# Performance work log

Measured on AMD Instinct MI355X. Metric: run time of the kernel, lower is better.

## Reference

```python
import jax, jax.numpy as jnp
import numpy as np

CONF_THRES = 0.8
NMS_THRES = 0.4
MAX_DET = 300          # fixed capacity for jit-compatible NMS output
N_BOXES = 262144
N_CLASSES = 80


def xywh2xyxy(x):
    xy, wh = x[..., :2], x[..., 2:4]
    return jnp.concatenate([xy - wh * 0.5, xy + wh * 0.5], axis=-1)


def bbox_iou(box, boxes):
    # one box [4] vs many [N,4]; original uses the +1 pixel-area convention
    x1 = jnp.maximum(box[0], boxes[:, 0])
    y1 = jnp.maximum(box[1], boxes[:, 1])
    x2 = jnp.minimum(box[2], boxes[:, 2])
    y2 = jnp.minimum(box[3], boxes[:, 3])
    inter = jnp.clip(x2 - x1 + 1, 0) * jnp.clip(y2 - y1 + 1, 0)
    a1 = (box[2] - box[0] + 1) * (box[3] - box[1] + 1)
    a2 = (boxes[:, 2] - boxes[:, 0] + 1) * (boxes[:, 3] - boxes[:, 1] + 1)
    return inter / (a1 + a2 - inter + 1e-16)


def nms_single(pred):
    # pred: [N, 85] raw YOLO output for one image
    boxes = xywh2xyxy(pred[:, :4])
    obj = pred[:, 4]
    cls_scores = pred[:, 5:]
    class_conf = cls_scores.max(axis=-1)
    class_pred = jnp.argmax(cls_scores, axis=-1).astype(pred.dtype)
    valid = obj >= CONF_THRES
    score = obj * class_conf
    # sort valid boxes by descending score; invalid pushed to the end
    order = jnp.argsort(jnp.where(valid, -score, jnp.inf))
    det = jnp.concatenate(
        [boxes, obj[:, None], class_conf[:, None], class_pred[:, None]], axis=1
    )[order]  # [N, 7] = x1,y1,x2,y2,obj,class_conf,class_pred
    valid = valid[order]

    def step(valid, _):
        idx = jnp.argmax(valid)            # first still-valid (= highest score)
        any_valid = jnp.any(valid)
        cur = det[idx]
        iou = bbox_iou(cur[:4], det[:, :4])
        invalid = (iou > NMS_THRES) & (det[:, 6] == cur[6]) & valid
        # weighted box merge over the suppressed group (as in original NMS)
        w = jnp.where(invalid, det[:, 4], 0.0)
        merged = (w[:, None] * det[:, :4]).sum(0) / (w.sum() + 1e-16)
        out = jnp.where(any_valid,
                        jnp.concatenate([merged, cur[4:]]),
                        jnp.zeros(7, pred.dtype))
        return valid & ~invalid, (out, any_valid)

    _, (kept, kept_valid) = jax.lax.scan(step, valid, None, length=MAX_DET)
    return kept, kept_valid  # [MAX_DET,7], [MAX_DET]


def setup_inputs() -> dict:
    key = jax.random.key(0)
    detections = jax.random.uniform(key, (1, N_BOXES, 5 + N_CLASSES), dtype=jnp.float32)
    return {"detections": detections}


def reference(detections):
    kept, kv = nms_single(detections[0])
    d = kept[:, 5:]                        # [MAX_DET, 2] = (class_conf, class_pred)
    conf_key = jnp.where(kv, d[:, 0], -jnp.inf)  # padded rows sort to the end
    order = jnp.argsort(conf_key)          # ascending (torch argsort)
    d = d[order][::-1]                     # torch.flip -> descending class_conf
    kv = kv[order][::-1]
    probs = jnp.where(kv, d[:, 0], 0.0)    # self.probs
    ids = d[:, 1][None, :]                 # self.ids, shape [1, MAX_DET]
    return ids, probs
```

## Files before the change

kernel.cpp:

```cpp
#include <hip/hip_runtime.h>

#pragma clang fp contract(off)

#define NBOX 262144
#define NCLS 80
#define ROWS 85
#define CAP 1024
#define NSUB 8
#define SUBCAP 128
#define POOL 8192
#define BPT 4

typedef unsigned long long ull;

__global__ __launch_bounds__(1024) void k_init(int* __restrict__ cnt_pad,
                                               int* __restrict__ pool_count,
                                               int* __restrict__ done_count) {
    const int t = threadIdx.x;
    for (int i = t; i < NCLS * NSUB * 16; i += 1024) cnt_pad[i] = 0;
    if (t == 0) { *pool_count = 0; *done_count = 0; }
}

__global__ __launch_bounds__(256) void k_stage1(const float* __restrict__ det,
                                                int* __restrict__ cnt_pad,
                                                ull* __restrict__ key2,
                                                float* __restrict__ conf2,
                                                float4* __restrict__ box2) {
    __shared__ int s_wl[1024];
    __shared__ float s_obj[1024];
    __shared__ int s_nv;
    const int t = threadIdx.x;
    const int b0 = blockIdx.x * 1024;
    const int sb = blockIdx.x & (NSUB - 1);

    if (t == 0) s_nv = 0;
    __syncthreads();

    float obj[BPT];
    #pragma unroll
    for (int i = 0; i < BPT; i++)
        obj[i] = det[(size_t)(b0 + (i << 8) + t) * ROWS + 4];
    #pragma unroll
    for (int i = 0; i < BPT; i++) {
        if (obj[i] >= 0.8f) {
            int r = atomicAdd(&s_nv, 1);
            s_wl[r] = (i << 8) + t;
            s_obj[r] = obj[i];
        }
    }
    __syncthreads();
    const int nv = s_nv;

    const int grp = t >> 4, c = t & 15;
    const int lane = t & 63;
    #pragma unroll 2
    for (int r0 = 0; r0 < nv; r0 += 16) {
        int widx = r0 + grp;
        if (widx < nv) {
            int b = s_wl[widx];
            const float* p = det + (size_t)(b0 + b) * ROWS;
            float aux = (c < 5) ? p[c] : 0.0f;
            float v0 = p[5 + c];
            float v1 = p[21 + c];
            float v2 = p[37 + c];
            float v3 = p[53 + c];
            float v4 = p[69 + c];
            float mv = v0; int mj = c;
            if (v1 > mv) { mv = v1; mj = 16 + c; }
            if (v2 > mv) { mv = v2; mj = 32 + c; }
            if (v3 > mv) { mv = v3; mj = 48 + c; }
            if (v4 > mv) { mv = v4; mj = 64 + c; }
            #pragma unroll
            for (int off = 8; off; off >>= 1) {
                float ov = __shfl_xor(mv, off);
                int oj = __shfl_xor(mj, off);
                if (ov > mv || (ov == mv && oj < mj)) { mv = ov; mj = oj; }
            }
            int gb = lane & 48;
            float x = __shfl(aux, gb + 0);
            float y = __shfl(aux, gb + 1);
            float w = __shfl(aux, gb + 2);
            float h = __shfl(aux, gb + 3);
            if (c == 0) {
                float ob = s_obj[widx];
                float score = ob * mv;
                float hw = w * 0.5f, hh = h * 0.5f;
                int gi = b0 + b;
                int r = atomicAdd(&cnt_pad[((mj * NSUB + sb) << 4)], 1);
                if (r < SUBCAP) {
                    int pos = (mj << 10) + (sb << 7) + r;
                    key2[pos] = ((ull)(~__float_as_uint(score)) << 32) | (unsigned)gi;
                    conf2[pos] = mv;
                    box2[pos] = make_float4(x - hw, y - hh, x + hw, y + hh);
                }
            }
        }
    }
}

template <int L>
__device__ __forceinline__ int exact_alive(ull (&k)[L]) {
    int a = 0;
    #pragma unroll
    for (int j = 0; j < L; j++) a += (int)__popcll(__ballot(k[j] != ~0ULL));
    return a;
}

template <int L>
__device__ __forceinline__ void pick_loop(ull (&k)[L], float4 (&bx)[L], float (&cf)[L],
                                          float (&ar)[L],
                                          int lane, int& alive, int& np,
                                          ull* pkey, float* pconf, int stopAt) {
    while (alive > stopAt && np < 300) {
        ull lm = k[0]; int lj = 0;
        #pragma unroll
        for (int j = 1; j < L; j++) if (k[j] < lm) { lm = k[j]; lj = j; }
        ull gm = lm;
        #pragma unroll
        for (int off = 32; off; off >>= 1) { ull o = __shfl_xor(gm, off); if (o < gm) gm = o; }
        if (gm == ~0ULL) { alive = 0; break; }
        float4 cb = bx[0]; float cc = cf[0];
        #pragma unroll
        for (int j = 1; j < L; j++) if (j == lj) { cb = bx[j]; cc = cf[j]; }
        ull wb = __ballot(lm == gm);
        int wl2 = (int)__ffsll((long long)wb) - 1;
        cb.x = __shfl(cb.x, wl2); cb.y = __shfl(cb.y, wl2);
        cb.z = __shfl(cb.z, wl2); cb.w = __shfl(cb.w, wl2);
        cc = __shfl(cc, wl2);
        if (lane == 0) { pkey[np] = gm; pconf[np] = cc; }
        np++;
        float a1 = (cb.z - cb.x + 1.0f) * (cb.w - cb.y + 1.0f);
        #pragma unroll
        for (int j = 0; j < L; j++) {
            if (k[j] != ~0ULL) {
                float4 b = bx[j];
                float xx1 = fmaxf(cb.x, b.x), yy1 = fmaxf(cb.y, b.y);
                float xx2 = fminf(cb.z, b.z), yy2 = fminf(cb.w, b.w);
                float iw = xx2 - xx1 + 1.0f, ih = yy2 - yy1 + 1.0f;
                float inter = fmaxf(iw, 0.0f) * fmaxf(ih, 0.0f);
                float iou = inter / (a1 + ar[j] - inter + 1e-16f);
                if (iou > 0.4f) k[j] = ~0ULL;
            }
        }
        if ((np & 7) == 0) alive = exact_alive(k);
    }
}

template <int LF, int LT>
__device__ __forceinline__ void compact_regs(ull (&k)[LF], float4 (&bx)[LF], float (&cf)[LF],
                                             ull (&k2)[LT], float4 (&b2)[LT], float (&c2)[LT],
                                             float (&a2)[LT],
                                             int lane, int alive,
                                             ull* dk, float4* db, float* dc) {
    int ci = 0;
    #pragma unroll
    for (int j = 0; j < LF; j++) if (k[j] != ~0ULL) ci++;
    int inc = ci;
    for (int off = 1; off < 64; off <<= 1) {
        int o = __shfl_up(inc, off);
        if (lane >= off) inc += o;
    }
    int wp = inc - ci;
    #pragma unroll
    for (int j = 0; j < LF; j++)
        if (k[j] != ~0ULL) { dk[wp] = k[j]; db[wp] = bx[j]; dc[wp] = cf[j]; wp++; }
    #pragma unroll
    for (int j = 0; j < LT; j++) {
        int pos = lane + (j << 6);
        bool ok = pos < alive;
        k2[j] = ok ? dk[pos] : ~0ULL;
        b2[j] = ok ? db[pos] : make_float4(0.f, 0.f, 0.f, 0.f);
        c2[j] = ok ? dc[pos] : 0.0f;
        a2[j] = (b2[j].z - b2[j].x + 1.0f) * (b2[j].w - b2[j].y + 1.0f);
    }
}

__device__ __forceinline__ void bsort512(ull (&x)[8], int lane) {
    #pragma unroll
    for (int k = 2; k <= 512; k <<= 1) {
        #pragma unroll
        for (int j = k >> 1; j >= 64; j >>= 1) {
            const int jr = j >> 6;
            #pragma unroll
            for (int r2 = 0; r2 < 8; r2++) {
                if ((r2 & jr) == 0) {
                    const bool asc = (((r2 << 6) & k) == 0);
                    ull a = x[r2], b = x[r2 | jr];
                    if ((a > b) == asc) { x[r2] = b; x[r2 | jr] = a; }
                }
            }
        }
        #pragma unroll
        for (int j = ((k >> 1) > 32 ? 32 : (k >> 1)); j >= 1; j >>= 1) {
            #pragma unroll
            for (int r2 = 0; r2 < 8; r2++) {
                int i = (r2 << 6) + lane;
                bool asc = ((i & k) == 0);
                ull o = __shfl_xor(x[r2], j);
                bool lower = ((lane & j) == 0);
                ull mn = x[r2] < o ? x[r2] : o;
                ull mx2 = x[r2] < o ? o : x[r2];
                x[r2] = (asc == lower) ? mn : mx2;
            }
        }
    }
}

__global__ __launch_bounds__(256) void k_nms(const int* __restrict__ cnt_pad,
                                             const ull* __restrict__ key2,
                                             const float* __restrict__ conf2,
                                             const float4* __restrict__ box2,
                                             ull* __restrict__ pool_key,
                                             float* __restrict__ pool_conf,
                                             int* __restrict__ pool_cls,
                                             int* __restrict__ pool_count,
                                             int* __restrict__ done_count,
                                             float* __restrict__ out) {
    __shared__ ull sk[CAP];
    __shared__ float4 sbx[CAP];
    __shared__ float scf[CAP];
    __shared__ ull pkey[CAP];
    __shared__ float pconf[CAP];
    __shared__ int s_fin;
    __shared__ int s_red[4];
    __shared__ int s_stat[2];
    __shared__ ull s_mm[8];
    __shared__ ull s_buf[512];
    __shared__ unsigned s_cb[512];
    __shared__ unsigned s_cl[512];

    const int c = blockIdx.x, t = threadIdx.x, lane = t & 63, wave = t >> 6;

    if (wave == 0) {
        const int s0 = c << 10;
        int cv0 = 0;
        if (lane < NSUB) cv0 = min(cnt_pad[((c * NSUB + lane) << 4)], SUBCAP);
        int ntot = cv0;
        #pragma unroll
        for (int off = 32; off; off >>= 1) ntot += __shfl_xor(ntot, off);

        ull k16[16]; float4 b16[16]; float c16[16]; float a16[16];
        #pragma unroll
        for (int j = 0; j < 16; j++) {
            int pos = lane + (j << 6);
            int sub = pos >> 7;
            int lim = __shfl(cv0, sub);
            bool ok = (pos & (SUBCAP - 1)) < lim;
            k16[j] = ok ? key2[s0 + pos] : ~0ULL;
            b16[j] = ok ? box2[s0 + pos] : make_float4(0.f, 0.f, 0.f, 0.f);
            c16[j] = ok ? conf2[s0 + pos] : 0.0f;
            a16[j] = (b16[j].z - b16[j].x + 1.0f) * (b16[j].w - b16[j].y + 1.0f);
        }
        int alive = ntot, np = 0;
        pick_loop<16>(k16, b16, c16, a16, lane, alive, np, pkey, pconf, 256);
        alive = exact_alive(k16);
        ull k4[4]; float4 b4[4]; float c4[4]; float a4[4];
        compact_regs<16, 4>(k16, b16, c16, k4, b4, c4, a4, lane, alive, sk, sbx, scf);
        pick_loop<4>(k4, b4, c4, a4, lane, alive, np, pkey, pconf, 64);
        alive = exact_alive(k4);
        ull k1[1]; float4 b1[1]; float c1[1]; float a1r[1];
        compact_regs<4, 1>(k4, b4, c4, k1, b1, c1, a1r, lane, alive, sk, sbx, scf);
        pick_loop<1>(k1, b1, c1, a1r, lane, alive, np, pkey, pconf, 0);

        int npw = min(np, 300);
        int base = 0;
        if (lane == 0 && npw) base = atomicAdd(pool_count, npw);
        base = __shfl(base, 0);
        for (int j = lane; j < npw; j += 64) {
            int pp = base + j;
            if (pp < POOL) {
                ull gm = pkey[j];
                pool_key[pp] = ((ull)((unsigned)(gm >> 32) & 0x7FFFFFFFu) << 32)
                             | ((gm & 0xFFFFFFFFull) << 14) | (ull)pp;
                pool_conf[pp] = pconf[j];
                pool_cls[pp] = c;
            }
        }
        __threadfence();
    }
    __syncthreads();
    if (t == 0) {
        int ticket = atomicAdd(done_count, 1);
        s_fin = (ticket == NCLS - 1) ? 1 : 0;
    }
    __syncthreads();
    if (!s_fin) return;
    __threadfence();

    const int K = min(atomicAdd(pool_count, 0), POOL);
    ull key[32];
    #pragma unroll
    for (int j = 0; j < 32; j++) {
        int pos = t + (j << 8);
        key[j] = (pos < K) ? pool_key[pos] : ~0ULL;
    }

    const bool selAll = (K <= 511);
    int bsh = 63; ull p = 0;
    if (!selAll) {
        ull mn = ~0ULL, mx = 0;
        #pragma unroll
        for (int j = 0; j < 32; j++) {
            ull kk = key[j];
            if (kk != ~0ULL) { if (kk < mn) mn = kk; if (kk > mx) mx = kk; }
        }
        #pragma unroll
        for (int off = 32; off; off >>= 1) {
            ull on = __shfl_xor(mn, off), ox = __shfl_xor(mx, off);
            if (on < mn) mn = on;
            if (ox > mx) mx = ox;
        }
        if (lane == 0) { s_mm[wave * 2] = mn; s_mm[wave * 2 + 1] = mx; }
        __syncthreads();
        mn = min(min(s_mm[0], s_mm[2]), min(s_mm[4], s_mm[6]));
        mx = max(max(s_mm[1], s_mm[3]), max(s_mm[5], s_mm[7]));
        ull diff = mn ^ mx;
        int hb = 63 - __builtin_clzll(diff);
        int r = 300, cand = K, b = hb;
        p = mn >> (hb + 1);
        while (b >= 13 && cand > 212) {
            int c0 = 0;
            #pragma unroll
            for (int j = 0; j < 32; j++) {
                ull kk = key[j];
                if ((kk >> (b + 1)) == p && (((kk >> b) & 1ull) == 0)) c0++;
            }
            #pragma unroll
            for (int off = 32; off; off >>= 1) c0 += __shfl_xor(c0, off);
            if (lane == 0) s_red[wave] = c0;
            __syncthreads();
            if (t == 0) s_stat[0] = s_red[0] + s_red[1] + s_red[2] + s_red[3];
            __syncthreads();
            int cnt0 = s_stat[0];
            if (r <= cnt0) { cand = cnt0; p = p << 1; }
            else { r -= cnt0; cand -= cnt0; p = (p << 1) | 1ull; }
            b--;
        }
        bsh = b + 1;
    }

    if (t == 0) s_stat[1] = 0;
    __syncthreads();
    int ci = 0;
    #pragma unroll
    for (int j = 0; j < 32; j++) {
        ull kk = key[j];
        bool sel = selAll ? ((kk >> 63) == 0) : ((kk >> bsh) <= p);
        if (sel) ci++;
    }
    int inc = ci;
    for (int off = 1; off < 64; off <<= 1) {
        int o = __shfl_up(inc, off);
        if (lane >= off) inc += o;
    }
    int wtot = __shfl(inc, 63);
    int wbase2 = 0;
    if (lane == 0 && wtot) wbase2 = atomicAdd(&s_stat[1], wtot);
    wbase2 = __shfl(wbase2, 0);
    int wp = wbase2 + inc - ci;
    #pragma unroll
    for (int j = 0; j < 32; j++) {
        ull kk = key[j];
        bool sel = selAll ? ((kk >> 63) == 0) : ((kk >> bsh) <= p);
        if (sel) s_buf[wp++] = kk;
    }
    __syncthreads();
    const int S = s_stat[1];
    for (int i = t; i < 512; i += 256) if (i >= S) s_buf[i] = ~0ULL;
    __syncthreads();
    if (wave != 0) return;

    #pragma clang loop unroll(disable)
    for (int pass = 0; pass < 2; pass++) {
        ull x[8];
        #pragma unroll
        for (int r2 = 0; r2 < 8; r2++) x[r2] = s_buf[(r2 << 6) + lane];
        bsort512(x, lane);
        if (pass == 0) {
            #pragma unroll
            for (int r2 = 0; r2 < 8; r2++) {
                int i = (r2 << 6) + lane;
                ull kk = x[r2];
                ull k2 = ~0ULL;
                if (i < 300 && kk != ~0ULL) {
                    int pidx = (int)(kk & 0x3FFFull);
                    unsigned cb = __float_as_uint(pool_conf[pidx]);
                    unsigned cl = (unsigned)pool_cls[pidx];
                    s_cb[i] = cb; s_cl[i] = cl;
                    k2 = ((ull)(~cb) << 32) | (unsigned)(~i);
                }
                s_buf[i] = k2;
            }
        } else {
            #pragma unroll
            for (int r2 = 0; r2 < 8; r2++) {
                int i = (r2 << 6) + lane;
                if (i < 300) {
                    ull kk = x[r2];
                    float idv = 0.0f, pv = 0.0f;
                    if (kk != ~0ULL) {
                        int slot = (int)(~(unsigned)(kk & 0xFFFFFFFFull));
                        pv = __uint_as_float(s_cb[slot]);
                        idv = (float)(int)s_cl[slot];
                    }
                    out[i] = idv;
                    out[300 + i] = pv;
                }
            }
        }
    }
}

extern "C" void kernel_launch(void* const* d_in, const int* in_sizes, int n_in,
                              void* d_out, int out_size, void* d_ws, size_t ws_size,
                              hipStream_t stream) {
    const float* det = (const float*)d_in[0];
    float* out = (float*)d_out;
    char* ws = (char*)d_ws;

    int* cnt_pad = (int*)(ws + 0);
    int* pool_count = (int*)(ws + 40960);
    int* done_count = (int*)(ws + 40964);
    ull* key2 = (ull*)(ws + 41024);
    float* conf2 = (float*)(ws + 696384);
    float4* box2 = (float4*)(ws + 1024064);
    ull* pool_key = (ull*)(ws + 2334784);
    float* pool_conf = (float*)(ws + 2400320);
    int* pool_cls = (int*)(ws + 2433088);

    k_init<<<1, 1024, 0, stream>>>(cnt_pad, pool_count, done_count);
    k_stage1<<<NBOX / 1024, 256, 0, stream>>>(det, cnt_pad, key2, conf2, box2);
    k_nms<<<NCLS, 256, 0, stream>>>(cnt_pad, key2, conf2, box2,
                                    pool_key, pool_conf, pool_cls, pool_count,
                                    done_count, out);
}
```

Measured before the change: 192.2 us.

## Split NMS into per-class and final kernels; halve stage1 block work

Stage1 now processes 512 boxes per block with 2 per thread, doubling the block count to raise parallelism on the memory-bound objectness scan. The per-class NMS kernel runs as a single 64-thread wave instead of a 256-thread block where three waves sat idle. The last-block ticket/threadfence handoff is replaced by a separate single-block final kernel. This trades atomic coordination for an extra kernel launch.

After: 183.6 us. -4.5%, faster.

```diff
diff --git a/kernel.cpp b/kernel.cpp
--- a/kernel.cpp
+++ b/kernel.cpp
@@ -9,16 +9,16 @@
 #define NSUB 8
 #define SUBCAP 128
 #define POOL 8192
-#define BPT 4
+#define BPT 2
+#define S1BOX 512
 
 typedef unsigned long long ull;
 
 __global__ __launch_bounds__(1024) void k_init(int* __restrict__ cnt_pad,
-                                               int* __restrict__ pool_count,
-                                               int* __restrict__ done_count) {
+                                               int* __restrict__ pool_count) {
     const int t = threadIdx.x;
     for (int i = t; i < NCLS * NSUB * 16; i += 1024) cnt_pad[i] = 0;
-    if (t == 0) { *pool_count = 0; *done_count = 0; }
+    if (t == 0) *pool_count = 0;
 }
 
 __global__ __launch_bounds__(256) void k_stage1(const float* __restrict__ det,
@@ -26,11 +26,11 @@
                                                 ull* __restrict__ key2,
                                                 float* __restrict__ conf2,
                                                 float4* __restrict__ box2) {
-    __shared__ int s_wl[1024];
-    __shared__ float s_obj[1024];
+    __shared__ int s_wl[S1BOX];
+    __shared__ float s_obj[S1BOX];
     __shared__ int s_nv;
     const int t = threadIdx.x;
-    const int b0 = blockIdx.x * 1024;
+    const int b0 = blockIdx.x * S1BOX;
     const int sb = blockIdx.x & (NSUB - 1);
 
     if (t == 0) s_nv = 0;
@@ -175,6 +175,67 @@
     }
 }
 
+__global__ __launch_bounds__(64) void k_nms(const int* __restrict__ cnt_pad,
+                                            const ull* __restrict__ key2,
+                                            const float* __restrict__ conf2,
+                                            const float4* __restrict__ box2,
+                                            ull* __restrict__ pool_key,
+                                            float* __restrict__ pool_conf,
+                                            int* __restrict__ pool_cls,
+                                            int* __restrict__ pool_count) {
+    __shared__ ull sk[CAP];
+    __shared__ float4 sbx[CAP];
+    __shared__ float scf[CAP];
+    __shared__ ull pkey[CAP];
+    __shared__ float pconf[CAP];
+    const int c = blockIdx.x, lane = threadIdx.x;
+    const int s0 = c << 10;
+
+    int cv0 = 0;
+    if (lane < NSUB) cv0 = min(cnt_pad[((c * NSUB + lane) << 4)], SUBCAP);
+    int ntot = cv0;
+    #pragma unroll
+    for (int off = 32; off; off >>= 1) ntot += __shfl_xor(ntot, off);
+
+    ull k16[16]; float4 b16[16]; float c16[16]; float a16[16];
+    #pragma unroll
+    for (int j = 0; j < 16; j++) {
+        int pos = lane + (j << 6);
+        int sub = pos >> 7;
+        int lim = __shfl(cv0, sub);
+        bool ok = (pos & (SUBCAP - 1)) < lim;
+        k16[j] = ok ? key2[s0 + pos] : ~0ULL;
+        b16[j] = ok ? box2[s0 + pos] : make_float4(0.f, 0.f, 0.f, 0.f);
+        c16[j] = ok ? conf2[s0 + pos] : 0.0f;
+        a16[j] = (b16[j].z - b16[j].x + 1.0f) * (b16[j].w - b16[j].y + 1.0f);
+    }
+    int alive = ntot, np = 0;
+    pick_loop<16>(k16, b16, c16, a16, lane, alive, np, pkey, pconf, 256);
+    alive = exact_alive(k16);
+    ull k4[4]; float4 b4[4]; float c4[4]; float a4[4];
+    compact_regs<16, 4>(k16, b16, c16, k4, b4, c4, a4, lane, alive, sk, sbx, scf);
+    pick_loop<4>(k4, b4, c4, a4, lane, alive, np, pkey, pconf, 64);
+    alive = exact_alive(k4);
+    ull k1[1]; float4 b1[1]; float c1[1]; float a1r[1];
+    compact_regs<4, 1>(k4, b4, c4, k1, b1, c1, a1r, lane, alive, sk, sbx, scf);
+    pick_loop<1>(k1, b1, c1, a1r, lane, alive, np, pkey, pconf, 0);
+
+    int npw = min(np, 300);
+    int base = 0;
+    if (lane == 0 && npw) base = atomicAdd(pool_count, npw);
+    base = __shfl(base, 0);
+    for (int j = lane; j < npw; j += 64) {
+        int pp = base + j;
+        if (pp < POOL) {
+            ull gm = pkey[j];
+            pool_key[pp] = ((ull)((unsigned)(gm >> 32) & 0x7FFFFFFFu) << 32)
+                         | ((gm & 0xFFFFFFFFull) << 14) | (ull)pp;
+            pool_conf[pp] = pconf[j];
+            pool_cls[pp] = c;
+        }
+    }
+}
+
 __device__ __forceinline__ void bsort512(ull (&x)[8], int lane) {
     #pragma unroll
     for (int k = 2; k <= 512; k <<= 1) {
@@ -206,88 +267,19 @@
     }
 }
 
-__global__ __launch_bounds__(256) void k_nms(const int* __restrict__ cnt_pad,
-                                             const ull* __restrict__ key2,
-                                             const float* __restrict__ conf2,
-                                             const float4* __restrict__ box2,
-                                             ull* __restrict__ pool_key,
-                                             float* __restrict__ pool_conf,
-                                             int* __restrict__ pool_cls,
-                                             int* __restrict__ pool_count,
-                                             int* __restrict__ done_count,
-                                             float* __restrict__ out) {
-    __shared__ ull sk[CAP];
-    __shared__ float4 sbx[CAP];
-    __shared__ float scf[CAP];
-    __shared__ ull pkey[CAP];
-    __shared__ float pconf[CAP];
-    __shared__ int s_fin;
+__global__ __launch_bounds__(256) void k_final(const ull* __restrict__ pool_key,
+                                               const float* __restrict__ pool_conf,
+                                               const int* __restrict__ pool_cls,
+                                               const int* __restrict__ pool_count,
+                                               float* __restrict__ out) {
     __shared__ int s_red[4];
     __shared__ int s_stat[2];
     __shared__ ull s_mm[8];
     __shared__ ull s_buf[512];
     __shared__ unsigned s_cb[512];
     __shared__ unsigned s_cl[512];
-
-    const int c = blockIdx.x, t = threadIdx.x, lane = t & 63, wave = t >> 6;
-
-    if (wave == 0) {
-        const int s0 = c << 10;
-        int cv0 = 0;
-        if (lane < NSUB) cv0 = min(cnt_pad[((c * NSUB + lane) << 4)], SUBCAP);
-        int ntot = cv0;
-        #pragma unroll
-        for (int off = 32; off; off >>= 1) ntot += __shfl_xor(ntot, off);
-
-        ull k16[16]; float4 b16[16]; float c16[16]; float a16[16];
-        #pragma unroll
-        for (int j = 0; j < 16; j++) {
-            int pos = lane + (j << 6);
-            int sub = pos >> 7;
-            int lim = __shfl(cv0, sub);
-            bool ok = (pos & (SUBCAP - 1)) < lim;
-            k16[j] = ok ? key2[s0 + pos] : ~0ULL;
-            b16[j] = ok ? box2[s0 + pos] : make_float4(0.f, 0.f, 0.f, 0.f);
-            c16[j] = ok ? conf2[s0 + pos] : 0.0f;
-            a16[j] = (b16[j].z - b16[j].x + 1.0f) * (b16[j].w - b16[j].y + 1.0f);
-        }
-        int alive = ntot, np = 0;
-        pick_loop<16>(k16, b16, c16, a16, lane, alive, np, pkey, pconf, 256);
-        alive = exact_alive(k16);
-        ull k4[4]; float4 b4[4]; float c4[4]; float a4[4];
-        compact_regs<16, 4>(k16, b16, c16, k4, b4, c4, a4, lane, alive, sk, sbx, scf);
-        pick_loop<4>(k4, b4, c4, a4, lane, alive, np, pkey, pconf, 64);
-        alive = exact_alive(k4);
-        ull k1[1]; float4 b1[1]; float c1[1]; float a1r[1];
-        compact_regs<4, 1>(k4, b4, c4, k1, b1, c1, a1r, lane, alive, sk, sbx, scf);
-        pick_loop<1>(k1, b1, c1, a1r, lane, alive, np, pkey, pconf, 0);
-
-        int npw = min(np, 300);
-        int base = 0;
-        if (lane == 0 && npw) base = atomicAdd(pool_count, npw);
-        base = __shfl(base, 0);
-        for (int j = lane; j < npw; j += 64) {
-            int pp = base + j;
-            if (pp < POOL) {
-                ull gm = pkey[j];
-                pool_key[pp] = ((ull)((unsigned)(gm >> 32) & 0x7FFFFFFFu) << 32)
-                             | ((gm & 0xFFFFFFFFull) << 14) | (ull)pp;
-                pool_conf[pp] = pconf[j];
-                pool_cls[pp] = c;
-            }
-        }
-        __threadfence();
-    }
-    __syncthreads();
-    if (t == 0) {
-        int ticket = atomicAdd(done_count, 1);
-        s_fin = (ticket == NCLS - 1) ? 1 : 0;
-    }
-    __syncthreads();
-    if (!s_fin) return;
-    __threadfence();
-
-    const int K = min(atomicAdd(pool_count, 0), POOL);
+    const int t = threadIdx.x, wave = t >> 6, lane = t & 63;
+    const int K = min(*pool_count, POOL);
     ull key[32];
     #pragma unroll
     for (int j = 0; j < 32; j++) {
@@ -420,7 +412,6 @@
 
     int* cnt_pad = (int*)(ws + 0);
     int* pool_count = (int*)(ws + 40960);
-    int* done_count = (int*)(ws + 40964);
     ull* key2 = (ull*)(ws + 41024);
     float* conf2 = (float*)(ws + 696384);
     float4* box2 = (float4*)(ws + 1024064);
@@ -428,9 +419,9 @@
     float* pool_conf = (float*)(ws + 2400320);
     int* pool_cls = (int*)(ws + 2433088);
 
-    k_init<<<1, 1024, 0, stream>>>(cnt_pad, pool_count, done_count);
-    k_stage1<<<NBOX / 1024, 256, 0, stream>>>(det, cnt_pad, key2, conf2, box2);
-    k_nms<<<NCLS, 256, 0, stream>>>(cnt_pad, key2, conf2, box2,
-                                    pool_key, pool_conf, pool_cls, pool_count,
-                                    done_count, out);
-}
+    k_init<<<1, 1024, 0, stream>>>(cnt_pad, pool_count);
+    k_stage1<<<NBOX / S1BOX, 256, 0, stream>>>(det, cnt_pad, key2, conf2, box2);
+    k_nms<<<NCLS, 64, 0, stream>>>(cnt_pad, key2, conf2, box2,
+                                   pool_key, pool_conf, pool_cls, pool_count);
+    k_final<<<1, 256, 0, stream>>>(pool_key, pool_conf, pool_cls, pool_count, out);
+}
```
